# Optimization experiments

Measured on AMD Instinct MI355X. Metric: run time of the kernel, lower is better.

The kernel has to match this reference:

```python
import jax, jax.numpy as jnp
import numpy as np

N = 50000      # nodes
E = 1600000    # message edges (avg degree 32)
EQ = 500000    # link-prediction query edges
IN, HID, OUT, FCH = 128, 128, 64, 256
ALPHA = 0.5


def setup_inputs() -> dict:
    key = jax.random.key(0)
    ks = jax.random.split(key, 8)
    def p(k, shape):
        fan_in = shape[0]
        return jax.random.normal(k, shape, jnp.float32) * (1.0 / np.sqrt(fan_in))
    return {
        "x": jax.random.normal(ks[0], (N, IN), jnp.float32),
        "edge_index": jax.random.randint(ks[1], (2, E), 0, N),
        "edge_label_index": jax.random.randint(ks[2], (2, EQ), 0, N),
        "W1": p(ks[3], (IN, HID)),  "b1": jnp.zeros((HID,), jnp.float32),
        "W2": p(ks[4], (HID, OUT)), "b2": jnp.zeros((OUT,), jnp.float32),
        "Wf1": p(ks[5], (IN, FCH)), "bf1": jnp.zeros((FCH,), jnp.float32),
        "Wf2": p(ks[6], (FCH, OUT)), "bf2": jnp.zeros((OUT,), jnp.float32),
    }


def reference(x, edge_index, edge_label_index, W1, b1, W2, b2, Wf1, bf1, Wf2, bf2):
    n = x.shape[0]
    # GCN self-loops + symmetric normalization (PyG GCNConv defaults)
    loop = jnp.arange(n)
    src = jnp.concatenate([edge_index[0], loop])
    dst = jnp.concatenate([edge_index[1], loop])
    deg = jax.ops.segment_sum(jnp.ones_like(dst, jnp.float32), dst, num_segments=n)
    dinv = jnp.where(deg > 0, jax.lax.rsqrt(deg), 0.0)
    norm = dinv[src] * dinv[dst]  # [E+N]

    def gcn(h, W, b):
        h = h @ W                                  # transform first (PyG order)
        msg = norm[:, None] * h[src]               # gather + scale per edge
        return jax.ops.segment_sum(msg, dst, num_segments=n) + b

    x_gcn = jax.nn.relu(gcn(x, W1, b1))
    x_gcn = gcn(x_gcn, W2, b2)
    x_fc = jax.nn.relu(x @ Wf1 + bf1) @ Wf2 + bf2
    z = x_gcn * (1.0 - ALPHA) + x_fc * ALPHA       # [N, OUT]
    # edge dot-product decode
    return jnp.sum(z[edge_label_index[0]] * z[edge_label_index[1]], axis=1)
```

## Files before the change

kernel.cpp:

```cpp
#include <hip/hip_runtime.h>

#define FIN   128
#define FHID  128
#define FOUT  64
#define FFC   256
#define CHUNK 4096
#define BKBITS 7
#define BKN   128
#define ECAP  4608

typedef __attribute__((ext_vector_type(8))) short          bf16x8;
typedef __attribute__((ext_vector_type(4))) float          f32x4;
typedef __attribute__((ext_vector_type(2))) float          f32x2;
typedef __attribute__((ext_vector_type(8))) unsigned short u16x8;

static __device__ __forceinline__ unsigned short f2bf(float f) {
    unsigned int u = __float_as_uint(f);
    u = (u + 0x7fffu + ((u >> 16) & 1u)) >> 16;
    return (unsigned short)u;
}
static __device__ __forceinline__ float bf2f(unsigned short s) {
    return __uint_as_float(((unsigned int)s) << 16);
}

__global__ __launch_bounds__(256) void cvt_binA_kernel(
    const float* __restrict__ x, const float* __restrict__ W1,
    const float* __restrict__ W2, const float* __restrict__ Wf1,
    const float* __restrict__ Wf2,
    unsigned short* __restrict__ xbf, unsigned short* __restrict__ w1t,
    unsigned short* __restrict__ w2t, unsigned short* __restrict__ wf1t,
    unsigned short* __restrict__ wf2t, long n4,
    const int* __restrict__ src, const int* __restrict__ dst,
    int* __restrict__ bcur, uint2* __restrict__ ebuf, int E, int NBA)
{
    int t = threadIdx.x;
    if (blockIdx.x < NBA) {
        __shared__ int hist[512];
        __shared__ int rstart[512];
        __shared__ int lcur[512];
        hist[t] = 0; hist[t + 256] = 0; lcur[t] = 0; lcur[t + 256] = 0;
        __syncthreads();
        int e0 = blockIdx.x * CHUNK;
        int e1 = min(e0 + CHUNK, E);
        for (int e = e0 + t; e < e1; e += 256)
            atomicAdd(&hist[dst[e] >> BKBITS], 1);
        __syncthreads();
        if (hist[t])       rstart[t]       = atomicAdd(&bcur[t],       hist[t]);
        if (hist[t + 256]) rstart[t + 256] = atomicAdd(&bcur[t + 256], hist[t + 256]);
        __syncthreads();
        for (int e = e0 + t; e < e1; e += 256) {
            int s = src[e], d = dst[e];
            int b = d >> BKBITS;
            int pos = rstart[b] + atomicAdd(&lcur[b], 1);
            if (pos < ECAP)
                ebuf[(size_t)b * ECAP + pos] = make_uint2((unsigned)s, (unsigned)d);
        }
        return;
    }
    long i = (long)(blockIdx.x - NBA) * 256 + t;
    if (i < 16384) {
        int k = (int)i >> 7, n = (int)i & 127;
        w1t[n * 128 + k] = f2bf(W1[i]);
    } else if (i < 24576) {
        int j = (int)i - 16384; int k = j >> 6, n = j & 63;
        w2t[n * 128 + k] = f2bf(W2[j]);
    } else if (i < 57344) {
        int j = (int)i - 24576; int k = j >> 8, n = j & 255;
        wf1t[n * 128 + k] = f2bf(Wf1[j]);
    } else if (i < 73728) {
        int j = (int)i - 57344; int k = j >> 6, n = j & 63;
        wf2t[n * 256 + k] = f2bf(Wf2[j]);
    } else if (i < 73728 + n4) {
        long j = i - 73728;
        float4 v = ((const float4*)x)[j];
        ushort4 o = make_ushort4(f2bf(v.x), f2bf(v.y), f2bf(v.z), f2bf(v.w));
        ((ushort4*)xbf)[j] = o;
    }
}

__global__ __launch_bounds__(256) void binB_kernel(
    const uint2* __restrict__ ebuf, const int* __restrict__ bcnt,
    int2* __restrict__ rp2, int* __restrict__ col, float* __restrict__ dinv,
    const unsigned short* __restrict__ xbf, unsigned char* __restrict__ xs,
    int N)
{
    __shared__ int cnt[128];
    __shared__ int tmp[256];
    __shared__ int ccur[128];
    __shared__ int scur[256];
    __shared__ float sdinv[128];
    __shared__ unsigned int skey[ECAP];
    int b = blockIdx.x;
    int t = threadIdx.x;
    size_t base = (size_t)b * ECAP;
    int ne = min(bcnt[b], ECAP);
    if (t < 128) cnt[t] = 0;
    scur[t] = 0;
    __syncthreads();
    for (int e = t; e < ne; e += 256) {
        uint2 ed = ebuf[base + e];
        atomicAdd(&cnt[ed.y & (BKN - 1)], 1);
        atomicAdd(&scur[ed.x >> 8], 1);
    }
    __syncthreads();
    int c = (t < 128) ? cnt[t] : 0;
    tmp[t] = c;
    __syncthreads();
    int acc = c;
    for (int off = 1; off < 128; off <<= 1) {
        int a = (t >= off) ? tmp[t - off] : 0;
        __syncthreads();
        acc += a; tmp[t] = acc;
        __syncthreads();
    }
    if (t < 128) {
        float di = rsqrtf((float)c + 1.0f);
        sdinv[t] = di;
        int node = b * BKN + t;
        int st = (int)base + acc - c;
        if (node < N) { dinv[node] = di; rp2[node] = make_int2(st, st + c); }
        ccur[t] = st;
    }
    __syncthreads();
    int sv = scur[t];
    tmp[t] = sv;
    __syncthreads();
    int sacc = sv;
    for (int off = 1; off < 256; off <<= 1) {
        int a = (t >= off) ? tmp[t - off] : 0;
        __syncthreads();
        sacc += a; tmp[t] = sacc;
        __syncthreads();
    }
    scur[t] = sacc - sv;
    __syncthreads();
    for (int e = t; e < ne; e += 256) {
        uint2 ed = ebuf[base + e];
        int pos = atomicAdd(&scur[ed.x >> 8], 1);
        skey[pos] = (ed.x << BKBITS) | (ed.y & (BKN - 1));
    }
    __syncthreads();
    for (int w = 0; w < ne; w += 256) {
        int e = w + t;
        if (e < ne) {
            unsigned int k = skey[e];
            int pos = atomicAdd(&ccur[k & (BKN - 1)], 1);
            col[pos] = (int)(k >> BKBITS);
        }
        __syncthreads();
    }
    int nl0 = t >> 3;
    int f0 = (t & 7) << 4;
    #pragma unroll
    for (int it = 0; it < 4; it++) {
        int nl = it * 32 + nl0;
        int gn = b * BKN + nl;
        if (gn >= N) continue;
        float d2 = sdinv[nl];
        const unsigned short* xr = xbf + (size_t)gn * FIN + f0;
        u16x8 v0 = *(const u16x8*)xr;
        u16x8 v1 = *(const u16x8*)(xr + 8);
        float f[16];
        #pragma unroll
        for (int j = 0; j < 8; j++) {
            f[j]     = d2 * bf2f((unsigned short)v0[j]);
            f[8 + j] = d2 * bf2f((unsigned short)v1[j]);
        }
        uint4 w;
        w.x = 0; w.y = 0; w.z = 0; w.w = 0;
        w.x = __builtin_amdgcn_cvt_pk_fp8_f32(f[0],  f[1],  w.x, false);
        w.x = __builtin_amdgcn_cvt_pk_fp8_f32(f[2],  f[3],  w.x, true);
        w.y = __builtin_amdgcn_cvt_pk_fp8_f32(f[4],  f[5],  w.y, false);
        w.y = __builtin_amdgcn_cvt_pk_fp8_f32(f[6],  f[7],  w.y, true);
        w.z = __builtin_amdgcn_cvt_pk_fp8_f32(f[8],  f[9],  w.z, false);
        w.z = __builtin_amdgcn_cvt_pk_fp8_f32(f[10], f[11], w.z, true);
        w.w = __builtin_amdgcn_cvt_pk_fp8_f32(f[12], f[13], w.w, false);
        w.w = __builtin_amdgcn_cvt_pk_fp8_f32(f[14], f[15], w.w, true);
        *(uint4*)(xs + (size_t)gn * 128 + f0) = w;
    }
}

__global__ __launch_bounds__(256) void fc_fused_kernel(
    const unsigned short* __restrict__ A,
    const unsigned short* __restrict__ B1T,
    const unsigned short* __restrict__ B2T,
    const float* __restrict__ bias1, const float* __restrict__ bias2,
    float* __restrict__ C, int M)
{
    __shared__ __align__(16) unsigned short lds[32768];
    const int tid  = threadIdx.x;
    const int lane = tid & 63;
    const int wave = tid >> 6;
    const int m = lane & 15;
    const int q = lane >> 4;
    const int rowbase = blockIdx.x * 64 + wave * 16;
    const int row = rowbase + m;

    #pragma unroll 4
    for (int i = tid; i < 4096; i += 256) {
        int ck = i >> 4, sl = i & 15;
        ((u16x8*)lds)[(ck << 4) | (sl ^ (ck & 7))] = ((const u16x8*)B1T)[i];
    }
    __syncthreads();

    f32x4 acc[16] = {};
    const unsigned short* arow = A + (size_t)row * FIN + q * 8;
    for (int k0 = 0; k0 < 128; k0 += 32) {
        bf16x8 a = {};
        if (row < M) a = *(const bf16x8*)(arow + k0);
        int sl = q + (k0 >> 3);
        #pragma unroll
        for (int c = 0; c < 16; c++) {
            int cc = c * 16 + m;
            bf16x8 b = ((const bf16x8*)lds)[(cc << 4) | (sl ^ (cc & 7))];
            acc[c] = __builtin_amdgcn_mfma_f32_16x16x32_bf16(a, b, acc[c], 0, 0, 0);
        }
    }
    __syncthreads();

    #pragma unroll 2
    for (int i = tid; i < 2048; i += 256) {
        int ck = i >> 5, sl = i & 31;
        ((u16x8*)lds)[2048 + ((ck << 5) | (sl ^ (ck & 7)))] = ((const u16x8*)B2T)[i];
    }
    #pragma unroll
    for (int c = 0; c < 16; c++) {
        int cc = c * 16 + m;
        float bv = bias1[cc];
        #pragma unroll
        for (int r = 0; r < 4; r++) {
            int rr = wave * 16 + q * 4 + r;
            float v = fmaxf(acc[c][r] + bv, 0.f);
            lds[rr * 256 + ((((cc >> 3) ^ (rr & 7)) << 3) | (cc & 7))] = f2bf(v);
        }
    }
    __syncthreads();

    f32x4 acc2[4] = {};
    {
        int rr = wave * 16 + m;
        for (int k0 = 0; k0 < 256; k0 += 32) {
            int sl = q + (k0 >> 3);
            bf16x8 a = ((const bf16x8*)lds)[(rr << 5) | (sl ^ (rr & 7))];
            #pragma unroll
            for (int c = 0; c < 4; c++) {
                int cc = c * 16 + m;
                bf16x8 b = ((const bf16x8*)lds)[2048 + ((cc << 5) | (sl ^ (cc & 7)))];
                acc2[c] = __builtin_amdgcn_mfma_f32_16x16x32_bf16(a, b, acc2[c], 0, 0, 0);
            }
        }
    }
    __syncthreads();

    constexpr int ROWB = 4 * 16 * 4 + 16;
    unsigned char* wbase = (unsigned char*)lds + wave * 16 * ROWB;
    #pragma unroll
    for (int c = 0; c < 4; c++) {
        int lc = c * 16 + m;
        float bv = bias2[lc];
        #pragma unroll
        for (int r = 0; r < 4; r++)
            ((float*)(wbase + (q * 4 + r) * ROWB))[lc] = acc2[c][r] + bv;
    }
    #pragma unroll
    for (int p = 0; p < 4; p++) {
        int r2 = p * 4 + (lane >> 4);
        int bo = (lane & 15) * 16;
        int gr = rowbase + r2;
        if (gr < M) {
            uint4 v = *(const uint4*)(wbase + r2 * ROWB + bo);
            *(uint4*)((unsigned char*)C + (size_t)gr * FOUT * 4 + bo) = v;
        }
    }
}

__global__ __launch_bounds__(256) void gcn_fused_kernel(
    const unsigned short* __restrict__ A,
    const unsigned short* __restrict__ B1T,
    const unsigned short* __restrict__ B2T,
    const float* __restrict__ bias1,
    const float* __restrict__ rowscale,
    unsigned short* __restrict__ C, int M)
{
    __shared__ __align__(16) unsigned short lds[24576];
    const int tid  = threadIdx.x;
    const int lane = tid & 63;
    const int wave = tid >> 6;
    const int m = lane & 15;
    const int q = lane >> 4;
    const int rowbase = blockIdx.x * 64 + wave * 16;
    const int row = rowbase + m;

    #pragma unroll 2
    for (int i = tid; i < 2048; i += 256) {
        int ck = i >> 4, sl = i & 15;
        ((u16x8*)lds)[(ck << 4) | (sl ^ (ck & 7))] = ((const u16x8*)B1T)[i];
    }
    #pragma unroll 2
    for (int i = tid; i < 1024; i += 256) {
        int ck = i >> 4, sl = i & 15;
        ((u16x8*)lds)[2048 + ((ck << 4) | (sl ^ (ck & 7)))] = ((const u16x8*)B2T)[i];
    }
    __syncthreads();

    f32x4 acc[8] = {};
    const unsigned short* arow = A + (size_t)row * FIN + q * 8;
    for (int k0 = 0; k0 < 128; k0 += 32) {
        bf16x8 a = {};
        if (row < M) a = *(const bf16x8*)(arow + k0);
        int sl = q + (k0 >> 3);
        #pragma unroll
        for (int c = 0; c < 8; c++) {
            int cc = c * 16 + m;
            bf16x8 b = ((const bf16x8*)lds)[(cc << 4) | (sl ^ (cc & 7))];
            acc[c] = __builtin_amdgcn_mfma_f32_16x16x32_bf16(a, b, acc[c], 0, 0, 0);
        }
    }
    __syncthreads();

    #pragma unroll
    for (int c = 0; c < 8; c++) {
        int cc = c * 16 + m;
        float bv = bias1[cc];
        #pragma unroll
        for (int r = 0; r < 4; r++) {
            int rr = wave * 16 + q * 4 + r;
            float v = fmaxf(acc[c][r] + bv, 0.f);
            lds[rr * 128 + ((((cc >> 3) ^ (rr & 7)) << 3) | (cc & 7))] = f2bf(v);
        }
    }
    __syncthreads();

    f32x4 acc2[4] = {};
    {
        int rr = wave * 16 + m;
        for (int k0 = 0; k0 < 128; k0 += 32) {
            int sl = q + (k0 >> 3);
            bf16x8 a = ((const bf16x8*)lds)[(rr << 4) | (sl ^ (rr & 7))];
            #pragma unroll
            for (int c = 0; c < 4; c++) {
                int cc = c * 16 + m;
                bf16x8 b = ((const bf16x8*)lds)[2048 + ((cc << 4) | (sl ^ (cc & 7)))];
                acc2[c] = __builtin_amdgcn_mfma_f32_16x16x32_bf16(a, b, acc2[c], 0, 0, 0);
            }
        }
    }
    float rs[4];
    #pragma unroll
    for (int r = 0; r < 4; r++) {
        int gr = rowbase + q * 4 + r;
        rs[r] = (gr < M) ? rowscale[gr] : 1.0f;
    }
    __syncthreads();

    constexpr int ROWB = 4 * 16 * 2 + 16;
    unsigned char* wbase = (unsigned char*)lds + wave * 16 * ROWB;
    #pragma unroll
    for (int c = 0; c < 4; c++) {
        int lc = c * 16 + m;
        #pragma unroll
        for (int r = 0; r < 4; r++)
            ((unsigned short*)(wbase + (q * 4 + r) * ROWB))[lc] =
                f2bf(acc2[c][r] * rs[r]);
    }
    #pragma unroll
    for (int p = 0; p < 2; p++) {
        int r2 = p * 8 + (lane >> 3);
        int bo = (lane & 7) * 16;
        int gr = rowbase + r2;
        if (gr < M) {
            uint4 v = *(const uint4*)(wbase + r2 * ROWB + bo);
            *(uint4*)((unsigned char*)C + (size_t)gr * FOUT * 2 + bo) = v;
        }
    }
}

__global__ __launch_bounds__(256) void pull1_kernel(
    const unsigned char* __restrict__ xs, const int2* __restrict__ rp2,
    const int* __restrict__ col, const float* __restrict__ dinv,
    unsigned short* __restrict__ aggx, int N)
{
    int tid = threadIdx.x;
    int node = blockIdx.x * 32 + (tid >> 3);
    if (node >= N) return;
    int f0 = (tid & 7) << 4;
    const unsigned char* base = xs + f0;
    float acc[16] = {};
    auto accum = [&](uint4 g) {
        f32x2 p;
        p = __builtin_amdgcn_cvt_pk_f32_fp8(g.x, false); acc[0]  += p.x; acc[1]  += p.y;
        p = __builtin_amdgcn_cvt_pk_f32_fp8(g.x, true);  acc[2]  += p.x; acc[3]  += p.y;
        p = __builtin_amdgcn_cvt_pk_f32_fp8(g.y, false); acc[4]  += p.x; acc[5]  += p.y;
        p = __builtin_amdgcn_cvt_pk_f32_fp8(g.y, true);  acc[6]  += p.x; acc[7]  += p.y;
        p = __builtin_amdgcn_cvt_pk_f32_fp8(g.z, false); acc[8]  += p.x; acc[9]  += p.y;
        p = __builtin_amdgcn_cvt_pk_f32_fp8(g.z, true);  acc[10] += p.x; acc[11] += p.y;
        p = __builtin_amdgcn_cvt_pk_f32_fp8(g.w, false); acc[12] += p.x; acc[13] += p.y;
        p = __builtin_amdgcn_cvt_pk_f32_fp8(g.w, true);  acc[14] += p.x; acc[15] += p.y;
    };
    accum(*(const uint4*)(base + (size_t)node * 128));
    int2 se = rp2[node];
    int e = se.x, end = se.y;
    for (; e + 4 <= end; e += 4) {
        int s0 = col[e], s1 = col[e + 1], s2 = col[e + 2], s3 = col[e + 3];
        uint4 g0 = *(const uint4*)(base + (size_t)s0 * 128);
        uint4 g1 = *(const uint4*)(base + (size_t)s1 * 128);
        uint4 g2 = *(const uint4*)(base + (size_t)s2 * 128);
        uint4 g3 = *(const uint4*)(base + (size_t)s3 * 128);
        accum(g0); accum(g1); accum(g2); accum(g3);
    }
    for (; e < end; e++)
        accum(*(const uint4*)(base + (size_t)col[e] * 128));
    float di = dinv[node];
    u16x8 o0, o1;
    #pragma unroll
    for (int j = 0; j < 8; j++) {
        o0[j] = f2bf(di * acc[j]);
        o1[j] = f2bf(di * acc[8 + j]);
    }
    *(u16x8*)(aggx + (size_t)node * FIN + f0)     = o0;
    *(u16x8*)(aggx + (size_t)node * FIN + f0 + 8) = o1;
}

__global__ __launch_bounds__(256) void pull2_kernel(
    const unsigned short* __restrict__ t2s, const int2* __restrict__ rp2,
    const int* __restrict__ col, const float* __restrict__ dinv,
    const float* __restrict__ xfc, const float* __restrict__ b2,
    unsigned short* __restrict__ zbf, int N)
{
    int tid = threadIdx.x;
    int node = blockIdx.x * 32 + (tid >> 3);
    if (node >= N) return;
    int f0 = (tid & 7) << 3;
    const unsigned short* base = t2s + f0;
    u16x8 own = *(const u16x8*)(base + (size_t)node * FOUT);
    float acc[8];
    #pragma unroll
    for (int j = 0; j < 8; j++) acc[j] = bf2f(own[j]);
    int2 se = rp2[node];
    int e = se.x, end = se.y;
    for (; e + 4 <= end; e += 4) {
        int s0 = col[e], s1 = col[e + 1], s2 = col[e + 2], s3 = col[e + 3];
        u16x8 v0 = *(const u16x8*)(base + (size_t)s0 * FOUT);
        u16x8 v1 = *(const u16x8*)(base + (size_t)s1 * FOUT);
        u16x8 v2 = *(const u16x8*)(base + (size_t)s2 * FOUT);
        u16x8 v3 = *(const u16x8*)(base + (size_t)s3 * FOUT);
        #pragma unroll
        for (int j = 0; j < 8; j++)
            acc[j] += (bf2f(v0[j]) + bf2f(v1[j])) + (bf2f(v2[j]) + bf2f(v3[j]));
    }
    for (; e < end; e++) {
        u16x8 v = *(const u16x8*)(base + (size_t)col[e] * FOUT);
        #pragma unroll
        for (int j = 0; j < 8; j++) acc[j] += bf2f(v[j]);
    }
    float di = dinv[node];
    float4 x0 = *(const float4*)(xfc + (size_t)node * FOUT + f0);
    float4 x1 = *(const float4*)(xfc + (size_t)node * FOUT + f0 + 4);
    float4 bb0 = *(const float4*)(b2 + f0);
    float4 bb1 = *(const float4*)(b2 + f0 + 4);
    float xf[8] = { x0.x, x0.y, x0.z, x0.w, x1.x, x1.y, x1.z, x1.w };
    float bv[8] = { bb0.x, bb0.y, bb0.z, bb0.w, bb1.x, bb1.y, bb1.z, bb1.w };
    u16x8 o;
    #pragma unroll
    for (int j = 0; j < 8; j++)
        o[j] = f2bf(0.5f * (di * acc[j] + bv[j]) + 0.5f * xf[j]);
    *(u16x8*)(zbf + (size_t)node * FOUT + f0) = o;
}

__global__ void decode_kernel(
    const unsigned short* __restrict__ zbf, const int* __restrict__ eli,
    float* __restrict__ out, int Q)
{
    int tid = blockIdx.x * blockDim.x + threadIdx.x;
    int q = tid >> 3;
    if (q >= Q) return;
    int lane = tid & 7;
    int a = eli[q];
    int b = eli[Q + q];
    u16x8 va = *(const u16x8*)(zbf + (size_t)a * FOUT + lane * 8);
    u16x8 vb = *(const u16x8*)(zbf + (size_t)b * FOUT + lane * 8);
    float s = 0.f;
    #pragma unroll
    for (int j = 0; j < 8; j++) s += bf2f(va[j]) * bf2f(vb[j]);
    s += __shfl_down(s, 4, 8);
    s += __shfl_down(s, 2, 8);
    s += __shfl_down(s, 1, 8);
    if (lane == 0) out[q] = s;
}

extern "C" void kernel_launch(void* const* d_in, const int* in_sizes, int n_in,
                              void* d_out, int out_size, void* d_ws, size_t ws_size,
                              hipStream_t stream)
{
    const float* x   = (const float*)d_in[0];
    const int*   ei  = (const int*)  d_in[1];
    const int*   eli = (const int*)  d_in[2];
    const float* W1  = (const float*)d_in[3];
    const float* b1  = (const float*)d_in[4];
    const float* W2  = (const float*)d_in[5];
    const float* b2  = (const float*)d_in[6];
    const float* Wf1 = (const float*)d_in[7];
    const float* bf1 = (const float*)d_in[8];
    const float* Wf2 = (const float*)d_in[9];
    const float* bf2 = (const float*)d_in[10];
    float* out = (float*)d_out;

    const int N = in_sizes[0] / FIN;
    const int E = in_sizes[1] / 2;
    const int Q = in_sizes[2] / 2;
    const int* src = ei;
    const int* dst = ei + E;
    const int NBK = (N + BKN - 1) >> BKBITS;
    const int NBA = (E + CHUNK - 1) / CHUNK;

    char* p = (char*)d_ws;
    float* dinv = (float*)p;             p += (size_t)N * 4;
    int2*  rp2  = (int2*)p;              p += (size_t)N * 8;
    int*   bcur = (int*)p;               p += 2048;
    unsigned short* xbf  = (unsigned short*)p; p += (size_t)N * FIN * 2;
    unsigned short* w1t  = (unsigned short*)p; p += FIN * FHID * 2;
    unsigned short* w2t  = (unsigned short*)p; p += FHID * FOUT * 2;
    unsigned short* wf1t = (unsigned short*)p; p += FIN * FFC * 2;
    unsigned short* wf2t = (unsigned short*)p; p += FFC * FOUT * 2;
    float* xfc = (float*)p;              p += (size_t)N * FOUT * 4;
    unsigned char* xs = (unsigned char*)p;     p += (size_t)N * 128;
    uint2* ebuf = (uint2*)p;             p += (size_t)NBK * ECAP * 8;
    int*   col  = (int*)p;               p += (size_t)NBK * ECAP * 4;
    unsigned short* aggx = (unsigned short*)p; p += (size_t)N * FIN * 2;
    unsigned short* t2s  = (unsigned short*)p; p += (size_t)N * FOUT * 2;
    unsigned short* zbf  = (unsigned short*)p; p += (size_t)N * FOUT * 2;

    const int TB = 256;

    hipMemsetAsync(bcur, 0, 2048, stream);

    {
        long n4 = (long)N * FIN / 4;
        long cvtThreads = 73728 + n4;
        int cvtBlocks = (int)((cvtThreads + TB - 1) / TB);
        cvt_binA_kernel<<<NBA + cvtBlocks, TB, 0, stream>>>(
            x, W1, W2, Wf1, Wf2, xbf, w1t, w2t, wf1t, wf2t, n4,
            src, dst, bcur, ebuf, E, NBA);
    }

    fc_fused_kernel<<<(N + 63) / 64, TB, 0, stream>>>(
        xbf, wf1t, wf2t, bf1, bf2, xfc, N);

    binB_kernel<<<NBK, TB, 0, stream>>>(ebuf, bcur, rp2, col, dinv, xbf, xs, N);

    pull1_kernel<<<(N + 31) / 32, TB, 0, stream>>>(xs, rp2, col, dinv, aggx, N);

    gcn_fused_kernel<<<(N + 63) / 64, TB, 0, stream>>>(
        aggx, w1t, w2t, b1, dinv, t2s, N);

    pull2_kernel<<<(N + 31) / 32, TB, 0, stream>>>(
        t2s, rp2, col, dinv, xfc, b2, zbf, N);

    {
        long total = (long)Q * 8;
        decode_kernel<<<(int)((total + TB - 1) / TB), TB, 0, stream>>>(
            zbf, eli, out, Q);
    }
}
```

Baseline: 254.4 us.

## Pack binned edges into 32-bit keys, double chunk size, and batch x conversion

Edge buffer entries shrink from an 8-byte (src,dst) pair to a 4-byte packed key (src<<7 | dst low bits), halving ebuf write and read traffic and removing the key construction in binB. The binning chunk per block doubles, so fewer blocks issue global bucket-cursor atomics. The x-to-bf16 conversion now has each thread handle four float4 elements, which cuts the conversion block count. The packed key relies on src fitting in 25 bits, which holds for N=50000.

```diff
diff --git a/kernel.cpp b/kernel.cpp
--- a/kernel.cpp
+++ b/kernel.cpp
@@ -4,7 +4,7 @@
 #define FHID  128
 #define FOUT  64
 #define FFC   256
-#define CHUNK 4096
+#define CHUNK 8192
 #define BKBITS 7
 #define BKN   128
 #define ECAP  4608
@@ -31,7 +31,7 @@
     unsigned short* __restrict__ w2t, unsigned short* __restrict__ wf1t,
     unsigned short* __restrict__ wf2t, long n4,
     const int* __restrict__ src, const int* __restrict__ dst,
-    int* __restrict__ bcur, uint2* __restrict__ ebuf, int E, int NBA)
+    int* __restrict__ bcur, unsigned int* __restrict__ ebuf, int E, int NBA)
 {
     int t = threadIdx.x;
     if (blockIdx.x < NBA) {
@@ -53,7 +53,8 @@
             int b = d >> BKBITS;
             int pos = rstart[b] + atomicAdd(&lcur[b], 1);
             if (pos < ECAP)
-                ebuf[(size_t)b * ECAP + pos] = make_uint2((unsigned)s, (unsigned)d);
+                ebuf[(size_t)b * ECAP + pos] =
+                    ((unsigned)s << BKBITS) | ((unsigned)d & (BKN - 1));
         }
         return;
     }
@@ -70,16 +71,25 @@
     } else if (i < 73728) {
         int j = (int)i - 57344; int k = j >> 6, n = j & 63;
         wf2t[n * 256 + k] = f2bf(Wf2[j]);
-    } else if (i < 73728 + n4) {
-        long j = i - 73728;
-        float4 v = ((const float4*)x)[j];
-        ushort4 o = make_ushort4(f2bf(v.x), f2bf(v.y), f2bf(v.z), f2bf(v.w));
-        ((ushort4*)xbf)[j] = o;
+    } else {
+        long xt = i - 73728;
+        long g = xt >> 8;
+        int  tt = (int)(xt & 255);
+        long b0 = g * 1024 + tt;
+        #pragma unroll
+        for (int k = 0; k < 4; k++) {
+            long idx = b0 + (long)k * 256;
+            if (idx < n4) {
+                float4 v = ((const float4*)x)[idx];
+                ushort4 o = make_ushort4(f2bf(v.x), f2bf(v.y), f2bf(v.z), f2bf(v.w));
+                ((ushort4*)xbf)[idx] = o;
+            }
+        }
     }
 }
 
 __global__ __launch_bounds__(256) void binB_kernel(
-    const uint2* __restrict__ ebuf, const int* __restrict__ bcnt,
+    const unsigned int* __restrict__ ebuf, const int* __restrict__ bcnt,
     int2* __restrict__ rp2, int* __restrict__ col, float* __restrict__ dinv,
     const unsigned short* __restrict__ xbf, unsigned char* __restrict__ xs,
     int N)
@@ -98,9 +108,9 @@
     scur[t] = 0;
     __syncthreads();
     for (int e = t; e < ne; e += 256) {
-        uint2 ed = ebuf[base + e];
-        atomicAdd(&cnt[ed.y & (BKN - 1)], 1);
-        atomicAdd(&scur[ed.x >> 8], 1);
+        unsigned int k = ebuf[base + e];
+        atomicAdd(&cnt[k & (BKN - 1)], 1);
+        atomicAdd(&scur[k >> 15], 1);
     }
     __syncthreads();
     int c = (t < 128) ? cnt[t] : 0;
@@ -135,9 +145,9 @@
     scur[t] = sacc - sv;
     __syncthreads();
     for (int e = t; e < ne; e += 256) {
-        uint2 ed = ebuf[base + e];
-        int pos = atomicAdd(&scur[ed.x >> 8], 1);
-        skey[pos] = (ed.x << BKBITS) | (ed.y & (BKN - 1));
+        unsigned int k = ebuf[base + e];
+        int pos = atomicAdd(&scur[k >> 15], 1);
+        skey[pos] = k;
     }
     __syncthreads();
     for (int w = 0; w < ne; w += 256) {
@@ -524,7 +534,7 @@
     unsigned short* wf2t = (unsigned short*)p; p += FFC * FOUT * 2;
     float* xfc = (float*)p;              p += (size_t)N * FOUT * 4;
     unsigned char* xs = (unsigned char*)p;     p += (size_t)N * 128;
-    uint2* ebuf = (uint2*)p;             p += (size_t)NBK * ECAP * 8;
+    unsigned int* ebuf = (unsigned int*)p;  p += (size_t)NBK * ECAP * 4;
     int*   col  = (int*)p;               p += (size_t)NBK * ECAP * 4;
     unsigned short* aggx = (unsigned short*)p; p += (size_t)N * FIN * 2;
     unsigned short* t2s  = (unsigned short*)p; p += (size_t)N * FOUT * 2;
@@ -536,7 +546,8 @@
 
     {
         long n4 = (long)N * FIN / 4;
-        long cvtThreads = 73728 + n4;
+        long xThreads = (n4 + 3) / 4;
+        long cvtThreads = 73728 + xThreads;
         int cvtBlocks = (int)((cvtThreads + TB - 1) / TB);
         cvt_binA_kernel<<<NBA + cvtBlocks, TB, 0, stream>>>(
             x, W1, W2, Wf1, Wf2, xbf, w1t, w2t, wf1t, wf2t, n4,
```

Result: no change. 257.1 us (+1.1%).
